# Performance work log

Measured on AMD Instinct MI355X. Metric: run time of the kernel, lower is better.

## Reference

```python
import jax, jax.numpy as jnp
import numpy as np

N_NODES = 30000
N_EDGES = 480000
F_IN = 64
F_EDGE = 16
HID = 128
N_LAYERS = 3
N_CLASSES = 10
MSG_EPS = 1e-7   # GENConv eps added after ReLU
SM_EPS = 1e-16   # PyG softmax denom eps
LN_EPS = 1e-5


def _layer_norm(x, g, b):
    m = jnp.mean(x, axis=-1, keepdims=True)
    v = jnp.mean((x - m) ** 2, axis=-1, keepdims=True)
    return (x - m) * jax.lax.rsqrt(v + LN_EPS) * g + b


def _gen_conv(h, ea, src, dst, t, w1, b1, lg, lb, w2, b2):
    # GENConv message: relu(x_j + e_ij) + eps  -> [E, H]
    msg = jax.nn.relu(h[src] + ea) + MSG_EPS
    # learnable-temperature segment softmax over incoming edges of each node
    logits = msg * t
    mx = jax.ops.segment_max(logits, dst, num_segments=N_NODES)
    e = jnp.exp(logits - mx[dst])
    s = jax.ops.segment_sum(e, dst, num_segments=N_NODES)
    alpha = e / (s[dst] + SM_EPS)
    agg = jax.ops.segment_sum(msg * alpha, dst, num_segments=N_NODES)  # [N, H]
    # out = MLP(aggr + x): Linear(H,2H) -> LayerNorm -> ReLU -> Linear(2H,H)
    z = agg + h
    z = jax.nn.relu(_layer_norm(z @ w1 + b1, lg, lb)) @ w2 + b2
    return z


def setup_inputs() -> dict:
    key = jax.random.key(0)
    ks = jax.random.split(key, 10)
    g = lambda k, s, sc=0.05: jax.random.normal(k, s, jnp.float32) * sc
    return {
        "x": g(ks[0], (N_NODES, F_IN), 1.0),
        "edge_attr": g(ks[1], (N_EDGES, F_EDGE), 1.0),
        "node_enc_w": g(ks[2], (F_IN, HID)),
        "node_enc_b": jnp.zeros((HID,), jnp.float32),
        "edge_enc_w": g(ks[3], (F_EDGE, HID)),
        "edge_enc_b": jnp.zeros((HID,), jnp.float32),
        "mlp1_w": g(ks[4], (N_LAYERS, HID, 2 * HID)),
        "mlp1_b": jnp.zeros((N_LAYERS, 2 * HID), jnp.float32),
        "mlp_ln_g": jnp.ones((N_LAYERS, 2 * HID), jnp.float32),
        "mlp_ln_b": jnp.zeros((N_LAYERS, 2 * HID), jnp.float32),
        "mlp2_w": g(ks[5], (N_LAYERS, 2 * HID, HID)),
        "mlp2_b": jnp.zeros((N_LAYERS, HID), jnp.float32),
        "t": jnp.ones((N_LAYERS,), jnp.float32),
        "norm_g": jnp.ones((N_LAYERS, HID), jnp.float32),
        "norm_b": jnp.zeros((N_LAYERS, HID), jnp.float32),
        "lin_w": g(ks[6], (HID, N_CLASSES)),
        "lin_b": jnp.zeros((N_CLASSES,), jnp.float32),
        "edge_index": jax.random.randint(ks[7], (2, N_EDGES), 0, N_NODES, jnp.int32),
    }


def reference(x, edge_attr, node_enc_w, node_enc_b, edge_enc_w, edge_enc_b,
              mlp1_w, mlp1_b, mlp_ln_g, mlp_ln_b, mlp2_w, mlp2_b, t,
              norm_g, norm_b, lin_w, lin_b, edge_index):
    src, dst = edge_index[0], edge_index[1]
    ea = edge_attr @ edge_enc_w + edge_enc_b   # [E, H]
    h = x @ node_enc_w + node_enc_b            # [N, H]
    # first layer applies the conv directly (as in the original forward)
    h = _gen_conv(h, ea, src, dst, t[0], mlp1_w[0], mlp1_b[0],
                  mlp_ln_g[0], mlp_ln_b[0], mlp2_w[0], mlp2_b[0])
    # remaining DeepGCN res+ layers: h = h + conv(dropout(relu(norm(h))))
    for i in range(1, N_LAYERS):
        res = h
        z = jax.nn.relu(_layer_norm(h, norm_g[i], norm_b[i]))  # dropout p=0.1 -> identity in eval
        z = _gen_conv(z, ea, src, dst, t[i], mlp1_w[i], mlp1_b[i],
                      mlp_ln_g[i], mlp_ln_b[i], mlp2_w[i], mlp2_b[i])
        h = z + res
    # final norm/act from layers[0] then classifier (dropout -> identity in eval)
    h = jax.nn.relu(_layer_norm(h, norm_g[0], norm_b[0]))
    return h @ lin_w + lin_b
```

## Files before the change

### kernel.cpp

```cpp
#include <hip/hip_runtime.h>
#include <hip/hip_bf16.h>

#define NN 30000
#define NE 480000
#define NROWT 1875

typedef __attribute__((ext_vector_type(8))) short short8;
typedef __attribute__((ext_vector_type(4))) float floatx4;

__device__ __forceinline__ short f2bs(float f) {
    __hip_bfloat16 h = __float2bfloat16(f);
    return *reinterpret_cast<short*>(&h);
}

__device__ __forceinline__ short2 split_bf16(float f) {
    __hip_bfloat16 h = __float2bfloat16(f);
    float r = f - __bfloat162float(h);
    __hip_bfloat16 l = __float2bfloat16(r);
    short2 out;
    out.x = *reinterpret_cast<short*>(&h);
    out.y = *reinterpret_cast<short*>(&l);
    return out;
}

__global__ void presplit_all(const float* __restrict__ ew, const float* __restrict__ nw,
                             const float* __restrict__ m1w, const float* __restrict__ m2w,
                             const float* __restrict__ lw,
                             short* __restrict__ ew_h, short* __restrict__ ew_l,
                             short* __restrict__ nw_h, short* __restrict__ nw_l,
                             short* __restrict__ m1_h, short* __restrict__ m1_l,
                             short* __restrict__ m2_h, short* __restrict__ m2_l,
                             short* __restrict__ lw_h, short* __restrict__ lw_l)
{
    int i = blockIdx.x * 256 + threadIdx.x;
    if (i < 2048) {
        int k = i >> 7, n = i & 127;
        short2 s = split_bf16(ew[i]);
        ew_h[n * 16 + k] = s.x; ew_l[n * 16 + k] = s.y;
    } else if (i < 10240) {
        int j = i - 2048;
        int k = j >> 7, n = j & 127;
        short2 s = split_bf16(nw[j]);
        nw_h[n * 64 + k] = s.x; nw_l[n * 64 + k] = s.y;
    } else if (i < 108544) {
        int j = i - 10240;
        int l = j >> 15, jj = j & 32767;
        int k = jj >> 8, n = jj & 255;
        short2 s = split_bf16(m1w[j]);
        m1_h[(size_t)l * 32768 + n * 128 + k] = s.x;
        m1_l[(size_t)l * 32768 + n * 128 + k] = s.y;
    } else if (i < 206848) {
        int j = i - 108544;
        int l = j >> 15, jj = j & 32767;
        int k = jj >> 7, n = jj & 127;
        short2 s = split_bf16(m2w[j]);
        m2_h[(size_t)l * 32768 + n * 256 + k] = s.x;
        m2_l[(size_t)l * 32768 + n * 256 + k] = s.y;
    } else if (i < 208896) {
        int j = i - 206848;
        int k = j >> 4, n = j & 15;
        short2 s = (n < 10) ? split_bf16(lw[k * 10 + n]) : short2{0, 0};
        lw_h[n * 128 + k] = s.x; lw_l[n * 128 + k] = s.y;
    }
}

template<int K, int N>
__launch_bounds__(256)
__global__ void gemm_a32(const float* __restrict__ A, const short* __restrict__ Bh,
                         const short* __restrict__ Bl, const float* __restrict__ bias,
                         float* __restrict__ C, unsigned* __restrict__ hp, int total_waves)
{
    int wave = ((blockIdx.x * 256) + threadIdx.x) >> 6;
    if (wave >= total_waves) return;
    constexpr int NT = N / 16;
    const int mt = wave / NT, nt = wave % NT;
    const int lane = threadIdx.x & 63;
    const int l15 = lane & 15, quad = lane >> 4;
    const int row = mt * 16 + l15;
    const int col = nt * 16 + l15;
    floatx4 acc = {0.f, 0.f, 0.f, 0.f};
#pragma unroll
    for (int k0 = 0; k0 < K; k0 += 32) {
        const int kb = k0 + quad * 8;
        short8 ah, al;
        const float* ap = A + (size_t)row * K + kb;
        floatx4 a0 = *(const floatx4*)ap;
        floatx4 a1 = *(const floatx4*)(ap + 4);
#pragma unroll
        for (int j = 0; j < 4; j++) {
            short2 s0 = split_bf16(a0[j]); ah[j] = s0.x; al[j] = s0.y;
            short2 s1 = split_bf16(a1[j]); ah[j + 4] = s1.x; al[j + 4] = s1.y;
        }
        short8 bh = *(const short8*)(Bh + (size_t)col * K + kb);
        short8 bl = *(const short8*)(Bl + (size_t)col * K + kb);
        acc = __builtin_amdgcn_mfma_f32_16x16x32_bf16(ah, bh, acc, 0, 0, 0);
        acc = __builtin_amdgcn_mfma_f32_16x16x32_bf16(al, bh, acc, 0, 0, 0);
        acc = __builtin_amdgcn_mfma_f32_16x16x32_bf16(ah, bl, acc, 0, 0, 0);
    }
    float bv = bias[col];
#pragma unroll
    for (int r = 0; r < 4; r++) {
        int ro = mt * 16 + quad * 4 + r;
        float v = acc[r] + bv;
        C[(size_t)ro * N + col] = v;
        int mb = (int)(unsigned short)f2bs(v);
        int ob = __shfl_xor(mb, 1, 64);
        if ((l15 & 1) == 0)
            hp[(size_t)ro * 64 + nt * 8 + (l15 >> 1)] = (unsigned)mb | ((unsigned)ob << 16);
    }
}

template<int K, int NTOT, int NTW, int NREAL>
__launch_bounds__(256)
__global__ void gemm_s(const short* __restrict__ Ah, const short* __restrict__ Al,
                       const short* __restrict__ Bh, const short* __restrict__ Bl,
                       const float* __restrict__ bias, float* __restrict__ C, int total_waves)
{
    int wave = ((blockIdx.x * 256) + threadIdx.x) >> 6;
    if (wave >= total_waves) return;
    constexpr int NG = NTOT / (16 * NTW);
    const int mt = wave / NG, g = wave % NG;
    const int lane = threadIdx.x & 63;
    const int l15 = lane & 15, quad = lane >> 4;
    const int row = mt * 16 + l15;
    floatx4 acc[NTW];
#pragma unroll
    for (int t = 0; t < NTW; t++) acc[t] = {0.f, 0.f, 0.f, 0.f};
#pragma unroll
    for (int k0 = 0; k0 < K; k0 += 32) {
        const int kb = k0 + quad * 8;
        short8 ah = *(const short8*)(Ah + (size_t)row * K + kb);
        short8 al = *(const short8*)(Al + (size_t)row * K + kb);
#pragma unroll
        for (int t = 0; t < NTW; t++) {
            int col = g * NTW * 16 + t * 16 + l15;
            short8 bh = *(const short8*)(Bh + (size_t)col * K + kb);
            short8 bl = *(const short8*)(Bl + (size_t)col * K + kb);
            acc[t] = __builtin_amdgcn_mfma_f32_16x16x32_bf16(ah, bh, acc[t], 0, 0, 0);
            acc[t] = __builtin_amdgcn_mfma_f32_16x16x32_bf16(al, bh, acc[t], 0, 0, 0);
            acc[t] = __builtin_amdgcn_mfma_f32_16x16x32_bf16(ah, bl, acc[t], 0, 0, 0);
        }
    }
#pragma unroll
    for (int t = 0; t < NTW; t++) {
        int col = g * NTW * 16 + t * 16 + l15;
        if (col < NREAL) {
            float bv = bias[col];
#pragma unroll
            for (int r = 0; r < 4; r++) {
                int ro = mt * 16 + quad * 4 + r;
                C[(size_t)ro * NREAL + col] = acc[t][r] + bv;
            }
        }
    }
}

__launch_bounds__(256)
__global__ void gemm_ea(const float* __restrict__ edge_attr, const int* __restrict__ eidx_csr,
                        const short* __restrict__ Bh, const short* __restrict__ Bl,
                        const float* __restrict__ bias, unsigned* __restrict__ ea4)
{
    __shared__ short tile[2][16][132];
    const int wv = threadIdx.x >> 6;
    const int sub = wv >> 1, g = wv & 1;
    const int lane = threadIdx.x & 63;
    const int l15 = lane & 15, quad = lane >> 4;
    const int p = blockIdx.x * 32 + sub * 16 + l15;
    short8 a;
    if (quad < 2) {
        int e = eidx_csr[p];
        const float* ap = edge_attr + (size_t)e * 16 + quad * 8;
        floatx4 a0 = *(const floatx4*)ap;
        floatx4 a1 = *(const floatx4*)(ap + 4);
#pragma unroll
        for (int j = 0; j < 4; j++) { a[j] = f2bs(a0[j]); a[j + 4] = f2bs(a1[j]); }
    } else {
#pragma unroll
        for (int j = 0; j < 8; j++) a[j] = 0;
    }
    floatx4 acc[4];
#pragma unroll
    for (int t = 0; t < 4; t++) acc[t] = {0.f, 0.f, 0.f, 0.f};
#pragma unroll
    for (int t = 0; t < 4; t++) {
        int col = g * 64 + t * 16 + l15;
        short8 bh, bl;
        if (quad < 2) {
            bh = *(const short8*)(Bh + (size_t)col * 16 + quad * 8);
            bl = *(const short8*)(Bl + (size_t)col * 16 + quad * 8);
        } else {
#pragma unroll
            for (int j = 0; j < 8; j++) { bh[j] = 0; bl[j] = 0; }
        }
        acc[t] = __builtin_amdgcn_mfma_f32_16x16x32_bf16(a, bh, acc[t], 0, 0, 0);
        acc[t] = __builtin_amdgcn_mfma_f32_16x16x32_bf16(a, bl, acc[t], 0, 0, 0);
    }
#pragma unroll
    for (int t = 0; t < 4; t++) {
        int col = g * 64 + t * 16 + l15;
        float bv = bias[col];
#pragma unroll
        for (int r = 0; r < 4; r++)
            tile[sub][quad * 4 + r][col] = f2bs(acc[t][r] + bv);
    }
    __syncthreads();
#pragma unroll
    for (int c = 0; c < 2; c++) {
        int idx = threadIdx.x + 256 * c;
        int o = idx * 16;
        int g4l = o >> 10;
        int lp = (o & 1023) >> 4;
        unsigned u[4];
#pragma unroll
        for (int e = 0; e < 4; e++) {
            int rl = g4l * 4 + e;
            u[e] = *(const unsigned*)&tile[rl >> 4][rl & 15][2 * lp];
        }
        uint4 val = make_uint4(u[0], u[1], u[2], u[3]);
        *(uint4*)((char*)ea4 + (size_t)blockIdx.x * 8192 + o) = val;
    }
}

__global__ void zero_kernel(int* __restrict__ p, int n)
{
    int i = blockIdx.x * 256 + threadIdx.x;
    if (i < n) p[i] = 0;
}

__global__ void hist_kernel(const int* __restrict__ dst, int* __restrict__ count)
{
    int e = blockIdx.x * 256 + threadIdx.x;
    if (e < NE) atomicAdd(count + dst[e], 1);
}

__launch_bounds__(1024)
__global__ void scan_kernel(const int* __restrict__ count, int* __restrict__ rowptr)
{
    __shared__ int part[1024];
    const int t = threadIdx.x;
    const int CH = (NN + 1023) / 1024;
    const int base = t * CH;
    int sum = 0;
    for (int j = 0; j < CH; j++) {
        int idx = base + j;
        if (idx < NN) sum += count[idx];
    }
    part[t] = sum;
    __syncthreads();
    for (int d = 1; d < 1024; d <<= 1) {
        int v = (t >= d) ? part[t - d] : 0;
        __syncthreads();
        part[t] += v;
        __syncthreads();
    }
    int off = (t == 0) ? 0 : part[t - 1];
    for (int j = 0; j < CH; j++) {
        int idx = base + j;
        if (idx < NN) { rowptr[idx] = off; off += count[idx]; }
    }
    if (t == 1023) rowptr[NN] = part[1023];
}

__global__ void scatter_kernel(const int* __restrict__ src, const int* __restrict__ dst,
                               const int* __restrict__ rowptr, int* __restrict__ cursor,
                               int* __restrict__ src_csr, int* __restrict__ eidx_csr)
{
    int e = blockIdx.x * 256 + threadIdx.x;
    if (e >= NE) return;
    int d = dst[e];
    int pos = rowptr[d] + atomicAdd(cursor + d, 1);
    src_csr[pos] = src[e];
    eidx_csr[pos] = e;
}

__device__ __forceinline__ void updm(float hv, float av, float tt, float m,
                                     float& s, float& n)
{
    float g = fmaxf(hv + av, 0.f) + 1e-7f;
    float e = __expf(g * tt) * m;
    s += e;
    n = fmaf(g, e, n);
}

__launch_bounds__(256)
__global__ void agg_kernel(const unsigned* __restrict__ hp, const float* __restrict__ hres,
                           const uint4* __restrict__ ea4q, const int* __restrict__ src_csr,
                           const int* __restrict__ rowptr, const float* __restrict__ tptr,
                           int layer, unsigned* __restrict__ Zp)
{
    int node = (blockIdx.x * 256 + threadIdx.x) >> 6;
    if (node >= NN) return;
    const int lane = threadIdx.x & 63;
    const float tt = tptr[layer];
    const int start = rowptr[node];
    const int end = rowptr[node + 1];
    const int g0 = start >> 2, g1 = (end + 3) >> 2;
    float S0[4] = {0.f, 0.f, 0.f, 0.f}, S1[4] = {0.f, 0.f, 0.f, 0.f};
    float N0[4] = {0.f, 0.f, 0.f, 0.f}, N1[4] = {0.f, 0.f, 0.f, 0.f};

#define PROC(GG, U)                                                                \
    {                                                                              \
        uint4 uu = ea4q[((size_t)(GG) << 6) + lane];                               \
        int4 sv = *(const int4*)(src_csr + 4 * (GG));                              \
        int jb = 4 * (GG);                                                         \
        float m0 = (jb     >= start && jb     < end) ? 1.f : 0.f;                  \
        float m1 = (jb + 1 >= start && jb + 1 < end) ? 1.f : 0.f;                  \
        float m2 = (jb + 2 >= start && jb + 2 < end) ? 1.f : 0.f;                  \
        float m3 = (jb + 3 >= start && jb + 3 < end) ? 1.f : 0.f;                  \
        unsigned ha = hp[(size_t)sv.x * 64 + lane];                                \
        unsigned hb = hp[(size_t)sv.y * 64 + lane];                                \
        unsigned hc = hp[(size_t)sv.z * 64 + lane];                                \
        unsigned hd = hp[(size_t)sv.w * 64 + lane];                                \
        updm(__uint_as_float(ha << 16), __uint_as_float(uu.x << 16), tt, m0, S0[U], N0[U]); \
        updm(__uint_as_float(ha & 0xffff0000u), __uint_as_float(uu.x & 0xffff0000u), tt, m0, S1[U], N1[U]); \
        updm(__uint_as_float(hb << 16), __uint_as_float(uu.y << 16), tt, m1, S0[U], N0[U]); \
        updm(__uint_as_float(hb & 0xffff0000u), __uint_as_float(uu.y & 0xffff0000u), tt, m1, S1[U], N1[U]); \
        updm(__uint_as_float(hc << 16), __uint_as_float(uu.z << 16), tt, m2, S0[U], N0[U]); \
        updm(__uint_as_float(hc & 0xffff0000u), __uint_as_float(uu.z & 0xffff0000u), tt, m2, S1[U], N1[U]); \
        updm(__uint_as_float(hd << 16), __uint_as_float(uu.w << 16), tt, m3, S0[U], N0[U]); \
        updm(__uint_as_float(hd & 0xffff0000u), __uint_as_float(uu.w & 0xffff0000u), tt, m3, S1[U], N1[U]); \
    }

    int g = g0;
    for (; g + 4 <= g1; g += 4) {
        PROC(g,     0);
        PROC(g + 1, 1);
        PROC(g + 2, 2);
        PROC(g + 3, 3);
    }
    for (; g < g1; g++) PROC(g, 0);
#undef PROC
    float s0 = (S0[0] + S0[1]) + (S0[2] + S0[3]);
    float s1 = (S1[0] + S1[1]) + (S1[2] + S1[3]);
    float n0 = (N0[0] + N0[1]) + (N0[2] + N0[3]);
    float n1 = (N1[0] + N1[1]) + (N1[2] + N1[3]);

    float2 res = ((const float2*)hres)[(size_t)node * 64 + lane];
    float ox = n0 / (s0 + 1e-16f) + res.x;
    float oy = n1 / (s1 + 1e-16f) + res.y;
    Zp[(size_t)node * 64 + lane] =
        (unsigned)(unsigned short)f2bs(ox) | ((unsigned)(unsigned short)f2bs(oy) << 16);
}

template<bool HAS_RES, bool FINAL>
__launch_bounds__(256)
__global__ void mlp_fused(const short* __restrict__ Ap,
                          const short* __restrict__ B1h, const short* __restrict__ B1l,
                          const float* __restrict__ b1, const float* __restrict__ g1,
                          const float* __restrict__ be1,
                          const short* __restrict__ B2h, const short* __restrict__ B2l,
                          const float* __restrict__ b2, const float* __restrict__ res,
                          const float* __restrict__ g2, const float* __restrict__ be2,
                          short* __restrict__ z1h,
                          float* __restrict__ Hout, float* __restrict__ HinOut,
                          unsigned* __restrict__ HP,
                          short* __restrict__ Fh, short* __restrict__ Fl)
{
    __shared__ __align__(16) short lds[32768];
    const int wv = threadIdx.x >> 6;
    const int lane = threadIdx.x & 63;
    const int l15 = lane & 15, quad = lane >> 4;
    const int tile = blockIdx.x * 4 + wv;
    const bool valid = (tile < NROWT);
    const int row = tile * 16 + l15;

    floatx4 acc[16];
#pragma unroll
    for (int t = 0; t < 16; t++) acc[t] = {0.f, 0.f, 0.f, 0.f};
    for (int hf = 0; hf < 2; hf++) {
        __syncthreads();
        {
            const float4* s1p = (const float4*)(B1h + hf * 16384);
            const float4* s2p = (const float4*)(B1l + hf * 16384);
            float4* d = (float4*)lds;
#pragma unroll
            for (int i = 0; i < 8; i++) {
                int t8 = threadIdx.x + 256 * i;
                int col = t8 >> 4, k8 = t8 & 15;
                int unit = col * 16 + (k8 ^ (col & 15));
                d[unit] = s1p[t8];
                d[2048 + unit] = s2p[t8];
            }
        }
        __syncthreads();
        if (valid) {
#pragma unroll
            for (int k0 = 0; k0 < 128; k0 += 32) {
                const int kb = k0 + quad * 8;
                const int kb8 = kb >> 3;
                short8 ah = *(const short8*)(Ap + (size_t)row * 128 + kb);
#pragma unroll
                for (int t = 0; t < 8; t++) {
                    int col = t * 16 + l15;
                    int unit = col * 16 + (kb8 ^ (col & 15));
                    const short* bp = lds + unit * 8;
                    short8 bh = *(const short8*)bp;
                    short8 bl = *(const short8*)(bp + 16384);
                    int ti = hf * 8 + t;
                    acc[ti] = __builtin_amdgcn_mfma_f32_16x16x32_bf16(ah, bh, acc[ti], 0, 0, 0);
                    acc[ti] = __builtin_amdgcn_mfma_f32_16x16x32_bf16(ah, bl, acc[ti], 0, 0, 0);
                }
            }
        }
    }
    if (valid) {
#pragma unroll
        for (int t = 0; t < 16; t++) {
            float bv = b1[t * 16 + l15];
#pragma unroll
            for (int r = 0; r < 4; r++) acc[t][r] += bv;
        }
        float s1[4] = {0.f, 0.f, 0.f, 0.f}, s2[4] = {0.f, 0.f, 0.f, 0.f};
#pragma unroll
        for (int t = 0; t < 16; t++)
#pragma unroll
            for (int r = 0; r < 4; r++) { s1[r] += acc[t][r]; s2[r] += acc[t][r] * acc[t][r]; }
#pragma unroll
        for (int m = 1; m <= 8; m <<= 1)
#pragma unroll
            for (int r = 0; r < 4; r++) {
                s1[r] += __shfl_xor(s1[r], m, 64);
                s2[r] += __shfl_xor(s2[r], m, 64);
            }
        float mean[4], rstd[4];
#pragma unroll
        for (int r = 0; r < 4; r++) {
            mean[r] = s1[r] * (1.f / 256.f);
            float var = s2[r] * (1.f / 256.f) - mean[r] * mean[r];
            rstd[r] = rsqrtf(var + 1e-5f);
        }
#pragma unroll
        for (int t = 0; t < 16; t++) {
            int col = t * 16 + l15;
            float gg = g1[col], bb = be1[col];
#pragma unroll
            for (int r = 0; r < 4; r++) {
                float y = fmaxf((acc[t][r] - mean[r]) * rstd[r] * gg + bb, 0.f);
                int ro = tile * 16 + quad * 4 + r;
                z1h[(size_t)ro * 256 + col] = f2bs(y);
            }
        }
    }
    floatx4 acc2[8];
#pragma unroll
    for (int t = 0; t < 8; t++) acc2[t] = {0.f, 0.f, 0.f, 0.f};
    for (int hf = 0; hf < 2; hf++) {
        __syncthreads();
        {
            const float4* s1p = (const float4*)(B2h + hf * 16384);
            const float4* s2p = (const float4*)(B2l + hf * 16384);
            float4* d = (float4*)lds;
#pragma unroll
            for (int i = 0; i < 8; i++) {
                int t8 = threadIdx.x + 256 * i;
                int col = t8 >> 5, k8 = t8 & 31;
                int unit = col * 32 + (k8 ^ (col & 15));
                d[unit] = s1p[t8];
                d[2048 + unit] = s2p[t8];
            }
        }
        __syncthreads();
        if (valid) {
#pragma unroll
            for (int k0 = 0; k0 < 256; k0 += 32) {
                const int kb = k0 + quad * 8;
                const int kb8 = kb >> 3;
                short8 zh = *(const short8*)(z1h + (size_t)row * 256 + kb);
#pragma unroll
                for (int t = 0; t < 4; t++) {
                    int col = t * 16 + l15;
                    int unit = col * 32 + (kb8 ^ (col & 15));
                    const short* bp = lds + unit * 8;
                    short8 bh = *(const short8*)bp;
                    short8 bl = *(const short8*)(bp + 16384);
                    int ti = hf * 4 + t;
                    acc2[ti] = __builtin_amdgcn_mfma_f32_16x16x32_bf16(zh, bh, acc2[ti], 0, 0, 0);
                    acc2[ti] = __builtin_amdgcn_mfma_f32_16x16x32_bf16(zh, bl, acc2[ti], 0, 0, 0);
                }
            }
        }
    }
    if (valid) {
#pragma unroll
        for (int t = 0; t < 8; t++) {
            int col = t * 16 + l15;
            float bv = b2[col];
#pragma unroll
            for (int r = 0; r < 4; r++) {
                acc2[t][r] += bv;
                if (HAS_RES) {
                    int ro = tile * 16 + quad * 4 + r;
                    acc2[t][r] += res[(size_t)ro * 128 + col];
                }
            }
        }
        float s1[4] = {0.f, 0.f, 0.f, 0.f}, s2[4] = {0.f, 0.f, 0.f, 0.f};
#pragma unroll
        for (int t = 0; t < 8; t++)
#pragma unroll
            for (int r = 0; r < 4; r++) { s1[r] += acc2[t][r]; s2[r] += acc2[t][r] * acc2[t][r]; }
#pragma unroll
        for (int m = 1; m <= 8; m <<= 1)
#pragma unroll
            for (int r = 0; r < 4; r++) {
                s1[r] += __shfl_xor(s1[r], m, 64);
                s2[r] += __shfl_xor(s2[r], m, 64);
            }
        float mean[4], rstd[4];
#pragma unroll
        for (int r = 0; r < 4; r++) {
            mean[r] = s1[r] * (1.f / 128.f);
            float var = s2[r] * (1.f / 128.f) - mean[r] * mean[r];
            rstd[r] = rsqrtf(var + 1e-5f);
        }
#pragma unroll
        for (int t = 0; t < 8; t++) {
            int col = t * 16 + l15;
            float gg = g2[col], bb = be2[col];
#pragma unroll
            for (int r = 0; r < 4; r++) {
                int ro = tile * 16 + quad * 4 + r;
                float x = acc2[t][r];
                float y = fmaxf((x - mean[r]) * rstd[r] * gg + bb, 0.f);
                if (FINAL) {
                    short2 sp = split_bf16(y);
                    Fh[(size_t)ro * 128 + col] = sp.x;
                    Fl[(size_t)ro * 128 + col] = sp.y;
                } else {
                    Hout[(size_t)ro * 128 + col] = x;
                    HinOut[(size_t)ro * 128 + col] = y;
                    int yb = (int)(unsigned short)f2bs(y);
                    int ob = __shfl_xor(yb, 1, 64);
                    if ((l15 & 1) == 0)
                        HP[(size_t)ro * 64 + t * 8 + (l15 >> 1)] =
                            (unsigned)yb | ((unsigned)ob << 16);
                }
            }
        }
    }
}

extern "C" void kernel_launch(void* const* d_in, const int* in_sizes, int n_in,
                              void* d_out, int out_size, void* d_ws, size_t ws_size,
                              hipStream_t stream)
{
    const float* x         = (const float*)d_in[0];
    const float* edge_attr = (const float*)d_in[1];
    const float* nw        = (const float*)d_in[2];
    const float* nb        = (const float*)d_in[3];
    const float* ew        = (const float*)d_in[4];
    const float* eb        = (const float*)d_in[5];
    const float* m1w       = (const float*)d_in[6];
    const float* m1b       = (const float*)d_in[7];
    const float* lng       = (const float*)d_in[8];
    const float* lnb       = (const float*)d_in[9];
    const float* m2w       = (const float*)d_in[10];
    const float* m2b       = (const float*)d_in[11];
    const float* tpr       = (const float*)d_in[12];
    const float* ng        = (const float*)d_in[13];
    const float* nbb       = (const float*)d_in[14];
    const float* lw        = (const float*)d_in[15];
    const float* lb        = (const float*)d_in[16];
    const int* ei  = (const int*)d_in[17];
    const int* src = ei;
    const int* dst = ei + NE;

    char* w = (char*)d_ws;
    unsigned* ea4 = (unsigned*)w; w += (size_t)NE * 128 * 2;
    int* src_csr  = (int*)w; w += (size_t)NE * 4;
    int* eidx_csr = (int*)w; w += (size_t)NE * 4;
    unsigned* hp  = (unsigned*)w; w += (size_t)NN * 64 * 4;
    unsigned* zp  = (unsigned*)w; w += (size_t)NN * 64 * 4;
    float* h   = (float*)w; w += (size_t)NN * 128 * 4;
    float* hin = (float*)w; w += (size_t)NN * 128 * 4;
    short* fin_h  = (short*)w; w += (size_t)NN * 128 * 2;
    short* fin_l  = (short*)w; w += (size_t)NN * 128 * 2;
    short* z1s_h  = (short*)w; w += (size_t)NN * 256 * 2;
    short* ew_h = (short*)w; w += (size_t)128 * 16 * 2;
    short* ew_l = (short*)w; w += (size_t)128 * 16 * 2;
    short* nw_h = (short*)w; w += (size_t)128 * 64 * 2;
    short* nw_l = (short*)w; w += (size_t)128 * 64 * 2;
    short* m1_h = (short*)w; w += (size_t)3 * 256 * 128 * 2;
    short* m1_l = (short*)w; w += (size_t)3 * 256 * 128 * 2;
    short* m2_h = (short*)w; w += (size_t)3 * 128 * 256 * 2;
    short* m2_l = (short*)w; w += (size_t)3 * 128 * 256 * 2;
    short* lw_h = (short*)w; w += (size_t)16 * 128 * 2;
    short* lw_l = (short*)w; w += (size_t)16 * 128 * 2;
    int* count  = (int*)w;   w += (size_t)NN * 4;
    int* cursor = (int*)w;   w += (size_t)NN * 4;
    int* rowptr = (int*)w;   w += (size_t)(NN + 1) * 4;

    zero_kernel<<<(2 * NN + 255) / 256, 256, 0, stream>>>(count, 2 * NN);
    hist_kernel<<<(NE + 255) / 256, 256, 0, stream>>>(dst, count);
    scan_kernel<<<1, 1024, 0, stream>>>(count, rowptr);
    scatter_kernel<<<(NE + 255) / 256, 256, 0, stream>>>(src, dst, rowptr, cursor,
                                                         src_csr, eidx_csr);

    presplit_all<<<(208896 + 255) / 256, 256, 0, stream>>>(
        ew, nw, m1w, m2w, lw, ew_h, ew_l, nw_h, nw_l, m1_h, m1_l, m2_h, m2_l, lw_h, lw_l);

    gemm_ea<<<NE / 32, 256, 0, stream>>>(edge_attr, eidx_csr, ew_h, ew_l, eb, ea4);
    gemm_a32<64, 128><<<(NN / 16) * 8 / 4, 256, 0, stream>>>(x, nw_h, nw_l, nb, h, hp,
                                                             (NN / 16) * 8);

    const uint4* ea4q = (const uint4*)ea4;
    const int mgrid = (NROWT + 3) / 4;
    for (int layer = 0; layer < 3; ++layer) {
        const float* hi = (layer == 0) ? h : hin;
        agg_kernel<<<NN / 4, 256, 0, stream>>>(hp, hi, ea4q, src_csr, rowptr, tpr, layer, zp);
        if (layer == 0) {
            mlp_fused<false, false><<<mgrid, 256, 0, stream>>>(
                (const short*)zp, m1_h, m1_l, m1b, lng, lnb,
                m2_h, m2_l, m2b, nullptr, ng + 128, nbb + 128,
                z1s_h, h, hin, hp, nullptr, nullptr);
        } else if (layer == 1) {
            mlp_fused<true, false><<<mgrid, 256, 0, stream>>>(
                (const short*)zp, m1_h + 32768, m1_l + 32768, m1b + 256, lng + 256, lnb + 256,
                m2_h + 32768, m2_l + 32768, m2b + 128, h, ng + 256, nbb + 256,
                z1s_h, h, hin, hp, nullptr, nullptr);
        } else {
            mlp_fused<true, true><<<mgrid, 256, 0, stream>>>(
                (const short*)zp, m1_h + 65536, m1_l + 65536, m1b + 512, lng + 512, lnb + 512,
                m2_h + 65536, m2_l + 65536, m2b + 256, h, ng, nbb,
                z1s_h, nullptr, nullptr, nullptr, fin_h, fin_l);
        }
    }
    gemm_s<128, 16, 1, 10><<<((NN / 16) + 3) / 4, 256, 0, stream>>>(
        fin_h, fin_l, lw_h, lw_l, lb, (float*)d_out, NN / 16);
}
```

Before: 487.9 us.

## Split each node's aggregation across two waves and double MLP block size

The aggregation kernel now assigns two wavefronts per node, each processing alternating edge groups, and combines their partial softmax sums through shared memory before writing. This aims to raise memory-level parallelism for the gather-heavy edge loop, but adds a block barrier and halves the number of nodes per block. Separately, the fused MLP kernel moves to 512-thread blocks covering 8 row tiles, so each staged weight tile in LDS serves twice as many rows. The larger blocks may reduce occupancy or leave a partially filled last block.

```diff
diff --git a/kernel.cpp b/kernel.cpp
--- a/kernel.cpp
+++ b/kernel.cpp
@@ -288,17 +288,19 @@
                            const int* __restrict__ rowptr, const float* __restrict__ tptr,
                            int layer, unsigned* __restrict__ Zp)
 {
-    int node = (blockIdx.x * 256 + threadIdx.x) >> 6;
-    if (node >= NN) return;
+    __shared__ float4 part[4][64];
+    const int wv = threadIdx.x >> 6;
+    const int node = blockIdx.x * 2 + (wv >> 1);
+    const int par = wv & 1;
     const int lane = threadIdx.x & 63;
     const float tt = tptr[layer];
     const int start = rowptr[node];
     const int end = rowptr[node + 1];
     const int g0 = start >> 2, g1 = (end + 3) >> 2;
-    float S0[4] = {0.f, 0.f, 0.f, 0.f}, S1[4] = {0.f, 0.f, 0.f, 0.f};
-    float N0[4] = {0.f, 0.f, 0.f, 0.f}, N1[4] = {0.f, 0.f, 0.f, 0.f};
-
-#define PROC(GG, U)                                                                \
+    float s0a = 0.f, s1a = 0.f, n0a = 0.f, n1a = 0.f;
+    float s0b = 0.f, s1b = 0.f, n0b = 0.f, n1b = 0.f;
+
+#define PROC(GG, S0, S1, N0, N1)                                                   \
     {                                                                              \
         uint4 uu = ea4q[((size_t)(GG) << 6) + lane];                               \
         int4 sv = *(const int4*)(src_csr + 4 * (GG));                              \
@@ -311,39 +313,40 @@
         unsigned hb = hp[(size_t)sv.y * 64 + lane];                                \
         unsigned hc = hp[(size_t)sv.z * 64 + lane];                                \
         unsigned hd = hp[(size_t)sv.w * 64 + lane];                                \
-        updm(__uint_as_float(ha << 16), __uint_as_float(uu.x << 16), tt, m0, S0[U], N0[U]); \
-        updm(__uint_as_float(ha & 0xffff0000u), __uint_as_float(uu.x & 0xffff0000u), tt, m0, S1[U], N1[U]); \
-        updm(__uint_as_float(hb << 16), __uint_as_float(uu.y << 16), tt, m1, S0[U], N0[U]); \
-        updm(__uint_as_float(hb & 0xffff0000u), __uint_as_float(uu.y & 0xffff0000u), tt, m1, S1[U], N1[U]); \
-        updm(__uint_as_float(hc << 16), __uint_as_float(uu.z << 16), tt, m2, S0[U], N0[U]); \
-        updm(__uint_as_float(hc & 0xffff0000u), __uint_as_float(uu.z & 0xffff0000u), tt, m2, S1[U], N1[U]); \
-        updm(__uint_as_float(hd << 16), __uint_as_float(uu.w << 16), tt, m3, S0[U], N0[U]); \
-        updm(__uint_as_float(hd & 0xffff0000u), __uint_as_float(uu.w & 0xffff0000u), tt, m3, S1[U], N1[U]); \
-    }
-
-    int g = g0;
-    for (; g + 4 <= g1; g += 4) {
-        PROC(g,     0);
-        PROC(g + 1, 1);
-        PROC(g + 2, 2);
-        PROC(g + 3, 3);
-    }
-    for (; g < g1; g++) PROC(g, 0);
+        updm(__uint_as_float(ha << 16), __uint_as_float(uu.x << 16), tt, m0, S0, N0); \
+        updm(__uint_as_float(ha & 0xffff0000u), __uint_as_float(uu.x & 0xffff0000u), tt, m0, S1, N1); \
+        updm(__uint_as_float(hb << 16), __uint_as_float(uu.y << 16), tt, m1, S0, N0); \
+        updm(__uint_as_float(hb & 0xffff0000u), __uint_as_float(uu.y & 0xffff0000u), tt, m1, S1, N1); \
+        updm(__uint_as_float(hc << 16), __uint_as_float(uu.z << 16), tt, m2, S0, N0); \
+        updm(__uint_as_float(hc & 0xffff0000u), __uint_as_float(uu.z & 0xffff0000u), tt, m2, S1, N1); \
+        updm(__uint_as_float(hd << 16), __uint_as_float(uu.w << 16), tt, m3, S0, N0); \
+        updm(__uint_as_float(hd & 0xffff0000u), __uint_as_float(uu.w & 0xffff0000u), tt, m3, S1, N1); \
+    }
+
+    int g = g0 + par;
+    for (; g + 2 < g1; g += 4) {
+        PROC(g, s0a, s1a, n0a, n1a);
+        PROC(g + 2, s0b, s1b, n0b, n1b);
+    }
+    if (g < g1) PROC(g, s0a, s1a, n0a, n1a);
 #undef PROC
-    float s0 = (S0[0] + S0[1]) + (S0[2] + S0[3]);
-    float s1 = (S1[0] + S1[1]) + (S1[2] + S1[3]);
-    float n0 = (N0[0] + N0[1]) + (N0[2] + N0[3]);
-    float n1 = (N1[0] + N1[1]) + (N1[2] + N1[3]);
-
-    float2 res = ((const float2*)hres)[(size_t)node * 64 + lane];
-    float ox = n0 / (s0 + 1e-16f) + res.x;
-    float oy = n1 / (s1 + 1e-16f) + res.y;
-    Zp[(size_t)node * 64 + lane] =
-        (unsigned)(unsigned short)f2bs(ox) | ((unsigned)(unsigned short)f2bs(oy) << 16);
+    float ps0 = s0a + s0b, ps1 = s1a + s1b, pn0 = n0a + n0b, pn1 = n1a + n1b;
+    part[wv][lane] = make_float4(ps0, ps1, pn0, pn1);
+    __syncthreads();
+    if (par == 0) {
+        float4 o = part[wv + 1][lane];
+        float s0 = ps0 + o.x, s1 = ps1 + o.y;
+        float n0 = pn0 + o.z, n1 = pn1 + o.w;
+        float2 res = ((const float2*)hres)[(size_t)node * 64 + lane];
+        float ox = n0 / (s0 + 1e-16f) + res.x;
+        float oy = n1 / (s1 + 1e-16f) + res.y;
+        Zp[(size_t)node * 64 + lane] =
+            (unsigned)(unsigned short)f2bs(ox) | ((unsigned)(unsigned short)f2bs(oy) << 16);
+    }
 }
 
 template<bool HAS_RES, bool FINAL>
-__launch_bounds__(256)
+__launch_bounds__(512)
 __global__ void mlp_fused(const short* __restrict__ Ap,
                           const short* __restrict__ B1h, const short* __restrict__ B1l,
                           const float* __restrict__ b1, const float* __restrict__ g1,
@@ -360,7 +363,7 @@
     const int wv = threadIdx.x >> 6;
     const int lane = threadIdx.x & 63;
     const int l15 = lane & 15, quad = lane >> 4;
-    const int tile = blockIdx.x * 4 + wv;
+    const int tile = blockIdx.x * 8 + wv;
     const bool valid = (tile < NROWT);
     const int row = tile * 16 + l15;
 
@@ -374,8 +377,8 @@
             const float4* s2p = (const float4*)(B1l + hf * 16384);
             float4* d = (float4*)lds;
 #pragma unroll
-            for (int i = 0; i < 8; i++) {
-                int t8 = threadIdx.x + 256 * i;
+            for (int i = 0; i < 4; i++) {
+                int t8 = threadIdx.x + 512 * i;
                 int col = t8 >> 4, k8 = t8 & 15;
                 int unit = col * 16 + (k8 ^ (col & 15));
                 d[unit] = s1p[t8];
@@ -451,8 +454,8 @@
             const float4* s2p = (const float4*)(B2l + hf * 16384);
             float4* d = (float4*)lds;
 #pragma unroll
-            for (int i = 0; i < 8; i++) {
-                int t8 = threadIdx.x + 256 * i;
+            for (int i = 0; i < 4; i++) {
+                int t8 = threadIdx.x + 512 * i;
                 int col = t8 >> 5, k8 = t8 & 31;
                 int unit = col * 32 + (k8 ^ (col & 15));
                 d[unit] = s1p[t8];
@@ -604,22 +607,22 @@
                                                              (NN / 16) * 8);
 
     const uint4* ea4q = (const uint4*)ea4;
-    const int mgrid = (NROWT + 3) / 4;
+    const int mgrid = (NROWT + 7) / 8;
     for (int layer = 0; layer < 3; ++layer) {
         const float* hi = (layer == 0) ? h : hin;
-        agg_kernel<<<NN / 4, 256, 0, stream>>>(hp, hi, ea4q, src_csr, rowptr, tpr, layer, zp);
+        agg_kernel<<<NN / 2, 256, 0, stream>>>(hp, hi, ea4q, src_csr, rowptr, tpr, layer, zp);
         if (layer == 0) {
-            mlp_fused<false, false><<<mgrid, 256, 0, stream>>>(
+            mlp_fused<false, false><<<mgrid, 512, 0, stream>>>(
                 (const short*)zp, m1_h, m1_l, m1b, lng, lnb,
                 m2_h, m2_l, m2b, nullptr, ng + 128, nbb + 128,
                 z1s_h, h, hin, hp, nullptr, nullptr);
         } else if (layer == 1) {
-            mlp_fused<true, false><<<mgrid, 256, 0, stream>>>(
+            mlp_fused<true, false><<<mgrid, 512, 0, stream>>>(
                 (const short*)zp, m1_h + 32768, m1_l + 32768, m1b + 256, lng + 256, lnb + 256,
                 m2_h + 32768, m2_l + 32768, m2b + 128, h, ng + 256, nbb + 256,
                 z1s_h, h, hin, hp, nullptr, nullptr);
         } else {
-            mlp_fused<true, true><<<mgrid, 256, 0, stream>>>(
+            mlp_fused<true, true><<<mgrid, 512, 0, stream>>>(
                 (const short*)zp, m1_h + 65536, m1_l + 65536, m1b + 512, lng + 512, lnb + 512,
                 m2_h + 65536, m2_l + 65536, m2b + 256, h, ng, nbb,
                 z1s_h, nullptr, nullptr, nullptr, fin_h, fin_l);
```

After: 492.7 us. About the same (+1.0%).
